# Kernel optimization log

Hardware: AMD Instinct MI355X
Metric: run time of the kernel (lower is better)

## Reference

```python
import jax, jax.numpy as jnp
import numpy as np

N_EMBD = 1024
N_HEAD = 16

def setup_inputs() -> dict:
    key = jax.random.key(0)
    k1, k2, k3 = jax.random.split(key, 3)
    x = jax.random.normal(k1, (2, 2048, N_EMBD), dtype=jnp.float32)
    # torch Linear(n, 3n): y = x @ W_attn (we store transposed weight directly)
    w_attn = jax.random.normal(k2, (N_EMBD, 3 * N_EMBD), dtype=jnp.float32) * 0.02
    w_proj = jax.random.normal(k3, (N_EMBD, N_EMBD), dtype=jnp.float32) * 0.02
    return {"x": x, "w_attn": w_attn, "w_proj": w_proj}

def reference(x, w_attn, w_proj):
    B, S, E = x.shape
    H = N_HEAD
    D = E // H
    qkv = x @ w_attn  # [B, S, 3E]
    q, k, v = jnp.split(qkv, 3, axis=-1)
    # [B, H, S, D]
    q = q.reshape(B, S, H, D).transpose(0, 2, 1, 3)
    k = k.reshape(B, S, H, D).transpose(0, 2, 1, 3)
    v = v.reshape(B, S, H, D).transpose(0, 2, 1, 3)
    scale = 1.0 / jnp.sqrt(jnp.asarray(D, dtype=x.dtype))
    a = jnp.einsum('bhqd,bhkd->bhqk', q, k) * scale  # [B, H, S, S]
    causal = jnp.tril(jnp.ones((S, S), dtype=bool))
    a = jnp.where(causal, a, -jnp.inf)
    a = jax.nn.softmax(a, axis=-1)
    y = jnp.einsum('bhqk,bhkd->bhqd', a, v)  # [B, H, S, D]
    y = y.transpose(0, 2, 1, 3).reshape(B, S, E)
    return y @ w_proj
```

## Files before the change

kernel.cpp:

```cpp
#include <hip/hip_runtime.h>

#define DEVI __device__ __forceinline__

typedef short bf16x8 __attribute__((ext_vector_type(8)));
typedef float f32x4 __attribute__((ext_vector_type(4)));
typedef unsigned short u16;
typedef unsigned int u32;

static constexpr int Bn = 2, S = 2048, E = 1024, H = 16, D = 64;
static constexpr int Mrows = Bn * S;
static constexpr int N_QKV = 3 * E;

DEVI u16 f2b(float f) {
  union { float f; u32 u; } c; c.f = f;
  return (u16)((c.u + 0x7FFFu + ((c.u >> 16) & 1u)) >> 16);
}

DEVI bf16x8 ld8(const u16* p) {
  union { uint4 u; bf16x8 v; } c;
  c.u = *reinterpret_cast<const uint4*>(p);
  return c.v;
}

#define MFMA(a, b, c) __builtin_amdgcn_mfma_f32_16x16x32_bf16(a, b, c, 0, 0, 0)

#define G2L16(gptr, lptr) \
  __builtin_amdgcn_global_load_lds((const __attribute__((address_space(1))) void*)(gptr), \
                                   (__attribute__((address_space(3))) void*)(lptr), 16, 0, 0)

__global__ __launch_bounds__(256) void prep(const float* __restrict__ x,
                                            const float* __restrict__ w_attn,
                                            const float* __restrict__ w_proj,
                                            u16* __restrict__ xb, u16* __restrict__ wabT,
                                            u16* __restrict__ wpbT) {
  __shared__ float t[32][33];
  int blk = blockIdx.x, tid = threadIdx.x;
  if (blk >= 4096) {
    int i = (blk - 4096) * 256 + tid;
    float4 f = reinterpret_cast<const float4*>(x)[i];
    ushort4 u;
    u.x = f2b(f.x); u.y = f2b(f.y); u.z = f2b(f.z); u.w = f2b(f.w);
    reinterpret_cast<ushort4*>(xb)[i] = u;
    return;
  }
  const float* in; u16* out; int R, C, bx, by;
  if (blk < 3072) {
    in = w_attn; out = wabT; R = E; C = N_QKV;
    bx = (blk % 96) * 32; by = (blk / 96) * 32;
  } else {
    int q = blk - 3072;
    in = w_proj; out = wpbT; R = E; C = E;
    bx = (q % 32) * 32; by = (q / 32) * 32;
  }
  int tx = tid & 31, ty = tid >> 5;
#pragma unroll
  for (int k = 0; k < 32; k += 8)
    t[ty + k][tx] = in[(size_t)(by + ty + k) * C + bx + tx];
  __syncthreads();
#pragma unroll
  for (int k = 0; k < 32; k += 8)
    out[(size_t)(bx + ty + k) * R + by + tx] = f2b(t[tx][ty + k]);
}

__global__ __launch_bounds__(256) void gemm_qkv(const u16* __restrict__ A, const u16* __restrict__ BT,
                                                u16* __restrict__ Qb, u16* __restrict__ Kb,
                                                u16* __restrict__ VbT) {
  constexpr int K = 1024, BK = 64;
  __shared__ __align__(16) u16 As[128 * BK];
  __shared__ __align__(16) u16 Bs[64 * BK];
  int tid = threadIdx.x;
  int w = tid >> 6, lane = tid & 63, quad = lane >> 4, l15 = lane & 15;
  int m0 = blockIdx.x * 128, n0 = blockIdx.y * 64;
  int mw = (w >> 1) * 64, nw = (w & 1) * 32;
  const u16* Ab = A + (size_t)m0 * K;
  const u16* Bb = BT + (size_t)n0 * K;
  f32x4 acc[4][2] = {};
  for (int k0 = 0; k0 < K; k0 += BK) {
#pragma unroll
    for (int j = 0; j < 4; j++) {
      int L = j * 256 + tid;
      int row = L >> 3, cg = (L & 7) ^ (row & 7);
      G2L16(Ab + (size_t)row * K + k0 + cg * 8, (char*)As + L * 16);
    }
#pragma unroll
    for (int j = 0; j < 2; j++) {
      int L = j * 256 + tid;
      int row = L >> 3, cg = (L & 7) ^ (row & 7);
      G2L16(Bb + (size_t)row * K + k0 + cg * 8, (char*)Bs + L * 16);
    }
    __syncthreads();
#pragma unroll
    for (int kk = 0; kk < 2; kk++) {
      int sg = ((kk << 2) | quad) ^ (l15 & 7);
      bf16x8 a[4], b[2];
#pragma unroll
      for (int i = 0; i < 4; i++) a[i] = ld8(&As[(mw + i * 16 + l15) * BK + sg * 8]);
#pragma unroll
      for (int i = 0; i < 2; i++) b[i] = ld8(&Bs[(nw + i * 16 + l15) * BK + sg * 8]);
#pragma unroll
      for (int mb = 0; mb < 4; mb++)
#pragma unroll
        for (int nb = 0; nb < 2; nb++)
          acc[mb][nb] = MFMA(a[mb], b[nb], acc[mb][nb]);
    }
    __syncthreads();
  }
#pragma unroll
  for (int mb = 0; mb < 4; mb++) {
    int m = m0 + mw + mb * 16 + quad * 4;
    int b = m >> 11, s = m & 2047;
#pragma unroll
    for (int nb = 0; nb < 2; nb++) {
      int n = n0 + nw + nb * 16 + l15;
      int sec = n >> 10, e = n & 1023, h = e >> 6, d = e & 63;
      int bh = b * H + h;
      if (sec == 0) {
#pragma unroll
        for (int r = 0; r < 4; r++)
          Qb[((size_t)bh * S + s + r) * D + d] = f2b(acc[mb][nb][r] * 0.1803368801111244f);
      } else if (sec == 1) {
#pragma unroll
        for (int r = 0; r < 4; r++)
          Kb[((size_t)bh * S + s + r) * D + d] = f2b(acc[mb][nb][r]);
      } else {
        ushort4 v;
        v.x = f2b(acc[mb][nb][0]); v.y = f2b(acc[mb][nb][1]);
        v.z = f2b(acc[mb][nb][2]); v.w = f2b(acc[mb][nb][3]);
        *reinterpret_cast<ushort4*>(VbT + ((size_t)bh * D + d) * S + s) = v;
      }
    }
  }
}

__global__ __launch_bounds__(256, 3) void attn(const u16* __restrict__ Qb, const u16* __restrict__ Kb,
                                               const u16* __restrict__ VbT, u16* __restrict__ Yb) {
  __shared__ __align__(16) u16 Ks[2][64 * 64];
  __shared__ __align__(16) u16 Vs[2][64 * 64];
  __shared__ __align__(16) u32 Ps[4][16 * 36];
  int w = threadIdx.x >> 6, lane = threadIdx.x & 63, quad = lane >> 4, l15 = lane & 15;
  int bh = blockIdx.x & 31, qt = 31 - (blockIdx.x >> 5);
  int b = bh >> 4, h = bh & 15;
  int nc = qt + 1;

  const u16* Kbh = Kb + (size_t)bh * S * D;
  const u16* Vbh = VbT + (size_t)bh * D * S;
  u32* myP = &Ps[w][0];
  const u16* myP16 = (const u16*)myP;

  int q_base = qt * 64 + w * 16;
  int qrow = q_base + l15;
  int kmax = q_base + 16;

  const u16* Qp = Qb + ((size_t)bh * S + qrow) * D + quad * 8;
  bf16x8 bq0 = ld8(Qp), bq1 = ld8(Qp + 32);

  float lpart = 0.f;
  f32x4 o[4] = {};

#pragma unroll
  for (int j = 0; j < 2; j++) {
    int L = (w * 2 + j) * 64 + lane;
    int row = L >> 3, cg = (L & 7) ^ (row & 7);
    G2L16(Kbh + (size_t)row * D + cg * 8, (char*)Ks[0] + L * 16);
  }
#pragma unroll
  for (int j = 0; j < 2; j++) {
    int L = (w * 2 + j) * 64 + lane;
    int row = L >> 3, cg = (L & 7) ^ (row & 7);
    G2L16(Vbh + (size_t)row * S + cg * 8, (char*)Vs[0] + L * 16);
  }

  for (int c = 0; c < nc; c++) {
    int kbase = c * 64;
    int cur = c & 1;
    if (c + 1 < nc) {
      const u16* Kg = Kbh + (size_t)(kbase + 64) * D;
      const u16* Vg = Vbh + (kbase + 64);
#pragma unroll
      for (int j = 0; j < 2; j++) {
        int L = (w * 2 + j) * 64 + lane;
        int row = L >> 3, cg = (L & 7) ^ (row & 7);
        G2L16(Kg + (size_t)row * D + cg * 8, (char*)Ks[cur ^ 1] + L * 16);
      }
#pragma unroll
      for (int j = 0; j < 2; j++) {
        int L = (w * 2 + j) * 64 + lane;
        int row = L >> 3, cg = (L & 7) ^ (row & 7);
        G2L16(Vg + (size_t)row * S + cg * 8, (char*)Vs[cur ^ 1] + L * 16);
      }
      asm volatile("s_waitcnt vmcnt(4)" ::: "memory");
    } else {
      asm volatile("s_waitcnt vmcnt(0)" ::: "memory");
    }
    __builtin_amdgcn_s_barrier();
    __builtin_amdgcn_sched_barrier(0);

    const u16* Kc = Ks[cur];
    const u16* Vc = Vs[cur];

#pragma unroll
    for (int mb = 0; mb < 4; mb++) {
      int kb = kbase + mb * 16;
      u32 pa = 0, pb = 0;
      if (kb < kmax) {
        int row = mb * 16 + l15;
        bf16x8 ak0 = ld8(&Kc[row * 64 + ((quad ^ (row & 7)) * 8)]);
        bf16x8 ak1 = ld8(&Kc[row * 64 + (((quad + 4) ^ (row & 7)) * 8)]);
        f32x4 z = {};
        __builtin_amdgcn_s_setprio(1);
        z = MFMA(ak0, bq0, z);
        z = MFMA(ak1, bq1, z);
        __builtin_amdgcn_s_setprio(0);
        if (kb == q_base) {
#pragma unroll
          for (int r = 0; r < 4; r++)
            if (quad * 4 + r > l15) z[r] = -1e30f;
        }
        float p0 = __builtin_amdgcn_exp2f(z[0]);
        float p1 = __builtin_amdgcn_exp2f(z[1]);
        float p2 = __builtin_amdgcn_exp2f(z[2]);
        float p3 = __builtin_amdgcn_exp2f(z[3]);
        lpart += (p0 + p1) + (p2 + p3);
        union { float f; u32 u; } c0, c1, c2, c3;
        c0.f = p0; c1.f = p1; c2.f = p2; c3.f = p3;
        pa = __builtin_amdgcn_perm(c1.u + 0x8000u, c0.u + 0x8000u, 0x07060302u);
        pb = __builtin_amdgcn_perm(c3.u + 0x8000u, c2.u + 0x8000u, 0x07060302u);
      }
      uint2 pw; pw.x = pa; pw.y = pb;
      *reinterpret_cast<uint2*>(&myP[l15 * 36 + quad * 2 + mb * 8]) = pw;
    }
#pragma unroll
    for (int ch = 0; ch < 2; ch++) {
      int kc = kbase + ch * 32;
      if (kc < kmax) {
        bf16x8 bp = ld8(myP16 + l15 * 72 + ch * 32 + quad * 8);
        __builtin_amdgcn_s_setprio(1);
#pragma unroll
        for (int dd = 0; dd < 4; dd++) {
          int rv = dd * 16 + l15;
          bf16x8 av = ld8(&Vc[rv * 64 + (((ch * 4 + quad) ^ (rv & 7)) * 8)]);
          o[dd] = MFMA(av, bp, o[dd]);
        }
        __builtin_amdgcn_s_setprio(0);
      }
    }
    asm volatile("s_waitcnt lgkmcnt(0)" ::: "memory");
    __builtin_amdgcn_s_barrier();
  }

  float l = lpart;
  l += __shfl_xor(l, 16);
  l += __shfl_xor(l, 32);
  float rinv = 1.0f / l;
  u16* Yp = Yb + ((size_t)b * S + qrow) * E + h * 64 + quad * 4;
#pragma unroll
  for (int dd = 0; dd < 4; dd++) {
    ushort4 y;
    y.x = f2b(o[dd][0] * rinv); y.y = f2b(o[dd][1] * rinv);
    y.z = f2b(o[dd][2] * rinv); y.w = f2b(o[dd][3] * rinv);
    *reinterpret_cast<ushort4*>(Yp + dd * 16) = y;
  }
}

__global__ __launch_bounds__(256) void gemm_proj(const u16* __restrict__ A, const u16* __restrict__ BT,
                                                 float* __restrict__ out) {
  constexpr int K = 1024, BK = 64;
  __shared__ __align__(16) u16 As[128 * BK];
  __shared__ __align__(16) u16 Bs[64 * BK];
  int tid = threadIdx.x;
  int w = tid >> 6, lane = tid & 63, quad = lane >> 4, l15 = lane & 15;
  int m0 = blockIdx.x * 128, n0 = blockIdx.y * 64;
  int mw = (w >> 1) * 64, nw = (w & 1) * 32;
  const u16* Ab = A + (size_t)m0 * K;
  const u16* Bb = BT + (size_t)n0 * K;
  f32x4 acc[4][2] = {};
  for (int k0 = 0; k0 < K; k0 += BK) {
#pragma unroll
    for (int j = 0; j < 4; j++) {
      int L = j * 256 + tid;
      int row = L >> 3, cg = (L & 7) ^ (row & 7);
      G2L16(Ab + (size_t)row * K + k0 + cg * 8, (char*)As + L * 16);
    }
#pragma unroll
    for (int j = 0; j < 2; j++) {
      int L = j * 256 + tid;
      int row = L >> 3, cg = (L & 7) ^ (row & 7);
      G2L16(Bb + (size_t)row * K + k0 + cg * 8, (char*)Bs + L * 16);
    }
    __syncthreads();
#pragma unroll
    for (int kk = 0; kk < 2; kk++) {
      int sg = ((kk << 2) | quad) ^ (l15 & 7);
      bf16x8 a[4], b[2];
#pragma unroll
      for (int i = 0; i < 4; i++) a[i] = ld8(&As[(mw + i * 16 + l15) * BK + sg * 8]);
#pragma unroll
      for (int i = 0; i < 2; i++) b[i] = ld8(&Bs[(nw + i * 16 + l15) * BK + sg * 8]);
#pragma unroll
      for (int mb = 0; mb < 4; mb++)
#pragma unroll
        for (int nb = 0; nb < 2; nb++)
          acc[mb][nb] = MFMA(a[mb], b[nb], acc[mb][nb]);
    }
    __syncthreads();
  }
#pragma unroll
  for (int mb = 0; mb < 4; mb++) {
    int m = m0 + mw + mb * 16 + quad * 4;
#pragma unroll
    for (int nb = 0; nb < 2; nb++) {
      int n = n0 + nw + nb * 16 + l15;
#pragma unroll
      for (int r = 0; r < 4; r++)
        out[(size_t)(m + r) * E + n] = acc[mb][nb][r];
    }
  }
}

extern "C" void kernel_launch(void* const* d_in, const int* in_sizes, int n_in,
                              void* d_out, int out_size, void* d_ws, size_t ws_size,
                              hipStream_t stream) {
  const float* x = (const float*)d_in[0];
  const float* w_attn = (const float*)d_in[1];
  const float* w_proj = (const float*)d_in[2];
  float* out = (float*)d_out;
  char* ws = (char*)d_ws;

  u16* xb   = (u16*)(ws);
  u16* wabT = (u16*)(ws + 8388608);
  u16* wpbT = (u16*)(ws + 14680064);
  u16* Qb   = (u16*)(ws + 16777216);
  u16* Kb   = (u16*)(ws + 25165824);
  u16* VbT  = (u16*)(ws + 33554432);
  u16* Yb   = (u16*)(ws + 41943040);

  prep<<<8192, 256, 0, stream>>>(x, w_attn, w_proj, xb, wabT, wpbT);
  gemm_qkv<<<dim3(Mrows / 128, N_QKV / 64), 256, 0, stream>>>(xb, wabT, Qb, Kb, VbT);
  attn<<<Bn * H * (S / 64), 256, 0, stream>>>(Qb, Kb, VbT, Yb);
  gemm_proj<<<dim3(Mrows / 128, E / 64), 256, 0, stream>>>(Yb, wpbT, out);
}
```

Before: 171.9 us.

## Keep softmax probabilities in registers and permute V reads to match layout

Removes the per-wave LDS staging buffer for P by packing the QK^T MFMA output directly into the B operand of the PV MFMA. V is read from LDS as two 8-byte halves whose k-index order matches the register-resident P layout. The q-tile-to-block mapping changes to a zigzag order that balances causal work, and launch bounds go up to 4 waves per SIMD. The cost is more, narrower LDS loads for V and possible register pressure under the tighter occupancy bound.

```diff
diff --git a/kernel.cpp b/kernel.cpp
--- a/kernel.cpp
+++ b/kernel.cpp
@@ -132,20 +132,20 @@
   }
 }
 
-__global__ __launch_bounds__(256, 3) void attn(const u16* __restrict__ Qb, const u16* __restrict__ Kb,
+__global__ __launch_bounds__(256, 4) void attn(const u16* __restrict__ Qb, const u16* __restrict__ Kb,
                                                const u16* __restrict__ VbT, u16* __restrict__ Yb) {
   __shared__ __align__(16) u16 Ks[2][64 * 64];
   __shared__ __align__(16) u16 Vs[2][64 * 64];
-  __shared__ __align__(16) u32 Ps[4][16 * 36];
   int w = threadIdx.x >> 6, lane = threadIdx.x & 63, quad = lane >> 4, l15 = lane & 15;
-  int bh = blockIdx.x & 31, qt = 31 - (blockIdx.x >> 5);
+  int bh = blockIdx.x & 31;
+  int g = blockIdx.x >> 5;
+  int ga = g & 7, gb = g >> 3;
+  int qt = ((gb & 2) << 3) + ((gb & 1) ? (15 - ga) : ga);
   int b = bh >> 4, h = bh & 15;
   int nc = qt + 1;
 
   const u16* Kbh = Kb + (size_t)bh * S * D;
   const u16* Vbh = VbT + (size_t)bh * D * S;
-  u32* myP = &Ps[w][0];
-  const u16* myP16 = (const u16*)myP;
 
   int q_base = qt * 64 + w * 16;
   int qrow = q_base + l15;
@@ -199,47 +199,51 @@
     const u16* Vc = Vs[cur];
 
 #pragma unroll
-    for (int mb = 0; mb < 4; mb++) {
-      int kb = kbase + mb * 16;
-      u32 pa = 0, pb = 0;
-      if (kb < kmax) {
-        int row = mb * 16 + l15;
-        bf16x8 ak0 = ld8(&Kc[row * 64 + ((quad ^ (row & 7)) * 8)]);
-        bf16x8 ak1 = ld8(&Kc[row * 64 + (((quad + 4) ^ (row & 7)) * 8)]);
-        f32x4 z = {};
-        __builtin_amdgcn_s_setprio(1);
-        z = MFMA(ak0, bq0, z);
-        z = MFMA(ak1, bq1, z);
-        __builtin_amdgcn_s_setprio(0);
-        if (kb == q_base) {
-#pragma unroll
-          for (int r = 0; r < 4; r++)
-            if (quad * 4 + r > l15) z[r] = -1e30f;
-        }
-        float p0 = __builtin_amdgcn_exp2f(z[0]);
-        float p1 = __builtin_amdgcn_exp2f(z[1]);
-        float p2 = __builtin_amdgcn_exp2f(z[2]);
-        float p3 = __builtin_amdgcn_exp2f(z[3]);
-        lpart += (p0 + p1) + (p2 + p3);
-        union { float f; u32 u; } c0, c1, c2, c3;
-        c0.f = p0; c1.f = p1; c2.f = p2; c3.f = p3;
-        pa = __builtin_amdgcn_perm(c1.u + 0x8000u, c0.u + 0x8000u, 0x07060302u);
-        pb = __builtin_amdgcn_perm(c3.u + 0x8000u, c2.u + 0x8000u, 0x07060302u);
-      }
-      uint2 pw; pw.x = pa; pw.y = pb;
-      *reinterpret_cast<uint2*>(&myP[l15 * 36 + quad * 2 + mb * 8]) = pw;
-    }
-#pragma unroll
     for (int ch = 0; ch < 2; ch++) {
       int kc = kbase + ch * 32;
       if (kc < kmax) {
-        bf16x8 bp = ld8(myP16 + l15 * 72 + ch * 32 + quad * 8);
+        u32 pw0 = 0, pw1 = 0, pw2 = 0, pw3 = 0;
+#pragma unroll
+        for (int s = 0; s < 2; s++) {
+          int kb = kc + s * 16;
+          if (kb < kmax) {
+            int row = (ch * 2 + s) * 16 + l15;
+            bf16x8 ak0 = ld8(&Kc[row * 64 + ((quad ^ (row & 7)) * 8)]);
+            bf16x8 ak1 = ld8(&Kc[row * 64 + (((quad + 4) ^ (row & 7)) * 8)]);
+            f32x4 z = {};
+            __builtin_amdgcn_s_setprio(1);
+            z = MFMA(ak0, bq0, z);
+            z = MFMA(ak1, bq1, z);
+            __builtin_amdgcn_s_setprio(0);
+            if (kb == q_base) {
+#pragma unroll
+              for (int r = 0; r < 4; r++)
+                if (quad * 4 + r > l15) z[r] = -1e30f;
+            }
+            float p0 = __builtin_amdgcn_exp2f(z[0]);
+            float p1 = __builtin_amdgcn_exp2f(z[1]);
+            float p2 = __builtin_amdgcn_exp2f(z[2]);
+            float p3 = __builtin_amdgcn_exp2f(z[3]);
+            lpart += (p0 + p1) + (p2 + p3);
+            union { float f; u32 u; } c0, c1, c2, c3;
+            c0.f = p0; c1.f = p1; c2.f = p2; c3.f = p3;
+            u32 pa = __builtin_amdgcn_perm(c1.u + 0x8000u, c0.u + 0x8000u, 0x07060302u);
+            u32 pb = __builtin_amdgcn_perm(c3.u + 0x8000u, c2.u + 0x8000u, 0x07060302u);
+            if (s == 0) { pw0 = pa; pw1 = pb; } else { pw2 = pa; pw3 = pb; }
+          }
+        }
+        union { u32 u[4]; bf16x8 v; } bp;
+        bp.u[0] = pw0; bp.u[1] = pw1; bp.u[2] = pw2; bp.u[3] = pw3;
+        int cg0 = ch * 4 + (quad >> 1), cg1 = cg0 + 2;
+        int woff = (quad & 1) * 4;
         __builtin_amdgcn_s_setprio(1);
 #pragma unroll
         for (int dd = 0; dd < 4; dd++) {
           int rv = dd * 16 + l15;
-          bf16x8 av = ld8(&Vc[rv * 64 + (((ch * 4 + quad) ^ (rv & 7)) * 8)]);
-          o[dd] = MFMA(av, bp, o[dd]);
+          union { uint2 d[2]; bf16x8 v; } av;
+          av.d[0] = *reinterpret_cast<const uint2*>(&Vc[rv * 64 + ((cg0 ^ (rv & 7)) * 8) + woff]);
+          av.d[1] = *reinterpret_cast<const uint2*>(&Vc[rv * 64 + ((cg1 ^ (rv & 7)) * 8) + woff]);
+          o[dd] = MFMA(av.v, bp.v, o[dd]);
         }
         __builtin_amdgcn_s_setprio(0);
       }
```

After: 177.4 us. 1.03x slower.
